# Kernel tuning notes

Measured on AMD Instinct MI355X. Metric: run time of the kernel, lower is better.

The kernel has to match this reference:

```python
import jax, jax.numpy as jnp
import numpy as np
import math

PI = math.pi
L = 6.0 * math.pi
EPS = 1e-5


def c19_activation(x, rho=4.0):
    scaled = x * (1.0 / PI)
    n = jnp.floor(scaled)
    t = scaled - n
    h = t * (1.0 - t)
    sgn = jnp.where(jnp.remainder(n, 2.0) < 1.0, 1.0, -1.0)
    core = PI * (sgn * h + rho * h * h)
    return jnp.where(x >= L, x - L, jnp.where(x <= -L, x + L, core))


def layer_norm(x, gamma, beta):
    mu = jnp.mean(x, axis=-1, keepdims=True)
    var = jnp.mean(jnp.square(x - mu), axis=-1, keepdims=True)
    return (x - mu) * jax.lax.rsqrt(var + EPS) * gamma + beta


def setup_inputs() -> dict:
    key = jax.random.key(0)
    ks = jax.random.split(key, 8)
    B, T, NB, D, DEPTH = 65536, 32, 8, 128, 4
    nl = DEPTH - 1  # 3 inner layers
    x = jax.random.normal(ks[0], (B, T, NB), dtype=jnp.float32)
    Wi = jax.random.normal(ks[1], (NB, D), dtype=jnp.float32) * 0.1   # input_proj (in, out)
    bi = jnp.zeros((D,), jnp.float32)
    Wo = jax.random.normal(ks[2], (D, NB), dtype=jnp.float32) * 0.1   # output_proj
    bo = jnp.zeros((NB,), jnp.float32)
    g_state = jnp.ones((D,), jnp.float32)
    b_state = jnp.zeros((D,), jnp.float32)
    Ws = jax.random.normal(ks[3], (nl, D, D), dtype=jnp.float32) * (1.0 / math.sqrt(D))
    bs = jnp.zeros((nl, D), jnp.float32)
    gs = jnp.ones((nl, D), jnp.float32)
    betas = jnp.zeros((nl, D), jnp.float32)
    return {"x": x, "Wi": Wi, "bi": bi, "Wo": Wo, "bo": bo,
            "g_state": g_state, "b_state": b_state,
            "Ws": Ws, "bs": bs, "gs": gs, "betas": betas}


def reference(x, Wi, bi, Wo, bo, g_state, b_state, Ws, bs, gs, betas):
    B, T, _ = x.shape
    D = Wi.shape[1]
    nl = Ws.shape[0]

    def step(h, xt):  # h: [B,D], xt: [B,NB]
        inp = xt @ Wi + bi
        state = 0.618 * layer_norm(h, g_state, b_state) + 0.382 * inp
        for i in range(nl):  # fixed small depth loop
            state = state + c19_activation(layer_norm(state, gs[i], betas[i]) @ Ws[i] + bs[i])
        out = state @ Wo + bo
        return state, out

    h0 = jnp.zeros((B, D), dtype=x.dtype)
    _, outs = jax.lax.scan(step, h0, jnp.swapaxes(x, 0, 1))  # outs: [T,B,NB]
    return jnp.swapaxes(outs, 0, 1)  # [B,T,NB]
```

## Files before the change

kernel.cpp:

```cpp
#include <hip/hip_runtime.h>
#include <math.h>

#define BDIM 512
#define BR   64
#define D    128
#define SPD  130
#define WSP  130
#define SWOP 12
#define TT   32
#define NB   8
#define NL   3

typedef double v4d __attribute__((ext_vector_type(4)));

__device__ __forceinline__ double c19_act_d(double x) {
    const double PI_D = 3.14159265358979323846;
    const double L6   = 6.0 * PI_D;
    double scaled = x * (1.0 / PI_D);
    double n = floor(scaled);
    double t = scaled - n;
    double h = t * (1.0 - t);
    double halfn = n * 0.5;
    double fr = halfn - floor(halfn);
    double sgn = (fr < 0.25) ? 1.0 : -1.0;
    double core = PI_D * (sgn * h + 4.0 * h * h);
    double r = core;
    r = (x <= -L6) ? (x + L6) : r;
    r = (x >=  L6) ? (x - L6) : r;
    return r;
}

__global__ void miniphi_prep(const float* __restrict__ Ws, const float* __restrict__ gs,
                             double* __restrict__ wp) {
    int idx = blockIdx.x * 256 + threadIdx.x;
    wp[idx] = (double)gs[idx >> 7] * (double)Ws[idx];
}

__global__ __launch_bounds__(BDIM) void miniphi_kernel(
    const float* __restrict__ x,  const float* __restrict__ Wi, const float* __restrict__ bi,
    const float* __restrict__ Wo, const float* __restrict__ bo,
    const float* __restrict__ g_state, const float* __restrict__ b_state,
    const float* __restrict__ Ws, const float* __restrict__ bs,
    const float* __restrict__ gs, const float* __restrict__ betas,
    const double* __restrict__ wp,
    float* __restrict__ out)
{
    __shared__ double sState[BR][SPD];
    __shared__ double sWq[2][32][WSP];
    __shared__ float  sWi[NB][D];
    __shared__ float  sWo[D][SWOP];
    __shared__ float  sBi[D], sGst[D], sBst[D];
    __shared__ double sGsD[NL][D];
    __shared__ double sGW[NL][D];
    __shared__ double sBWbs[NL][D];
    __shared__ double sRstd[BR], sMu2[BR];
    __shared__ float  sBo[NB];
    __shared__ int    sPR[64][4], sPC[64][4];
    __shared__ int    sFlag;

    const int tid  = threadIdx.x;
    const int lane = tid & 63;
    const int wv   = tid >> 6;

    for (int i = tid; i < NB * D; i += BDIM) sWi[i >> 7][i & 127] = Wi[i];
    for (int i = tid; i < D * NB; i += BDIM) sWo[i >> 3][i & 7] = Wo[i];
    for (int i = tid; i < D; i += BDIM) { sBi[i] = bi[i]; sGst[i] = g_state[i]; sBst[i] = b_state[i]; }
    for (int i = tid; i < NL * D; i += BDIM) sGsD[i >> 7][i & 127] = (double)gs[i];
    if (tid < NB) sBo[tid] = bo[tid];
    for (int i = tid; i < BR * D; i += BDIM) sState[i >> 7][i & 127] = 0.0;
    if (tid < NL * D) {
        int ly = tid >> 7, c = tid & 127;
        const float* wl = Ws + (size_t)ly * D * D;
        double gw = 0.0, bw = 0.0;
        for (int k = 0; k < D; ++k) {
            double w = (double)wl[k * D + c];
            gw = fma((double)gs[ly * D + k], w, gw);
            bw = fma((double)betas[ly * D + k], w, bw);
        }
        sGW[ly][c] = gw;
        sBWbs[ly][c] = bw + (double)bs[ly * D + c];
    }

    if (wv == 0) {
        const int lm = lane & 15, lk = lane >> 4;
        v4d z = {0.0, 0.0, 0.0, 0.0};
        v4d p1 = __builtin_amdgcn_mfma_f64_16x16x4f64((double)lm, 1.0, z, 0, 0, 0);
        v4d p2 = __builtin_amdgcn_mfma_f64_16x16x4f64(1.0, (double)lm, z, 0, 0, 0);
        double pk = (double)(1 << lk);
        v4d p3 = __builtin_amdgcn_mfma_f64_16x16x4f64(pk, pk, z, 0, 0, 0);
        v4d p4 = __builtin_amdgcn_mfma_f64_16x16x4f64(1.0 + 0x1p-30, 1.0, z, 0, 0, 0);
        double pa5 = (lk == 0) ? 1.0 : 0x1p-52;
        v4d p5 = __builtin_amdgcn_mfma_f64_16x16x4f64(pa5, 1.0, z, 0, 0, 0);
        bool ok = true;
        #pragma unroll
        for (int i = 0; i < 4; ++i) {
            double v = p1[i]; int r = (int)(v * 0.25 + 0.5);
            ok = ok && (v == 4.0 * (double)r) && (r >= 0) && (r < 16);
            sPR[lane][i] = r;
            double w = p2[i]; int c2 = (int)(w * 0.25 + 0.5);
            ok = ok && (w == 4.0 * (double)c2) && (c2 >= 0) && (c2 < 16);
            sPC[lane][i] = c2;
            ok = ok && (p3[i] == 85.0);
            ok = ok && (p4[i] == 4.0 + 0x1p-28);
            ok = ok && (p5[i] == 1.0 + 3.0 * 0x1p-52);
        }
        unsigned long long bal = __ballot(ok ? 1 : 0);
        if (lane == 0) sFlag = (bal == 0xFFFFFFFFFFFFFFFFull) ? 1 : 0;
    }
    __syncthreads();

    const int useMfma = sFlag;
    int pr[4], pc[4];
    #pragma unroll
    for (int i = 0; i < 4; ++i) { pr[i] = sPR[lane][i]; pc[i] = sPC[lane][i]; }

    const int rLN = tid >> 3;
    const int sL  = tid & 7;
    const int lm  = lane & 15, lk = lane >> 4;
    const int n0  = wv * 16;
    const int r0v = wv * 8;
    const size_t rowg = (size_t)blockIdx.x * BR;

    #define STAGE_Q(LY, Q, QB)                                                      \
      { if (wp) {                                                                   \
          const double* src = wp + (((size_t)(LY) * D + (Q) * 32) * D);             \
          _Pragma("unroll")                                                         \
          for (int i_ = 0; i_ < 4; ++i_) {                                          \
              int kr_ = wv * 4 + i_;                                                \
              const double* g_ = src + (size_t)kr_ * D + lane * 2;                  \
              __builtin_amdgcn_global_load_lds(                                     \
                  (const __attribute__((address_space(1))) void*)g_,                \
                  (__attribute__((address_space(3))) void*)&sWq[QB][kr_][0],        \
                  16, 0, 0);                                                        \
          }                                                                         \
        } else {                                                                    \
          const float* src = Ws + (((size_t)(LY) * D + (Q) * 32) * D);              \
          const double* gl = &sGsD[LY][(Q) * 32];                                   \
          _Pragma("unroll")                                                         \
          for (int i_ = 0; i_ < 4; ++i_) {                                          \
              int kr_ = wv * 4 + i_;                                                \
              float2 w_ = *(const float2*)(src + (size_t)kr_ * D + lane * 2);       \
              double g_ = gl[kr_];                                                  \
              double2 o_; o_.x = g_ * (double)w_.x; o_.y = g_ * (double)w_.y;       \
              *(double2*)&sWq[QB][kr_][lane * 2] = o_;                              \
          }                                                                         \
        } }

    #define GEMM_Q(QB, QK)                                                          \
      if (useMfma) {                                                                \
          _Pragma("unroll")                                                         \
          for (int k0 = 0; k0 < 32; k0 += 4) {                                      \
              double b  = sWq[QB][k0 + lk][n0 + lm];                                \
              double a0 = sState[lm     ][(QK) + k0 + lk];                          \
              double a1 = sState[lm + 16][(QK) + k0 + lk];                          \
              double a2 = sState[lm + 32][(QK) + k0 + lk];                          \
              double a3 = sState[lm + 48][(QK) + k0 + lk];                          \
              acc0 = __builtin_amdgcn_mfma_f64_16x16x4f64(a0, b, acc0, 0, 0, 0);    \
              acc1 = __builtin_amdgcn_mfma_f64_16x16x4f64(a1, b, acc1, 0, 0, 0);    \
              acc2 = __builtin_amdgcn_mfma_f64_16x16x4f64(a2, b, acc2, 0, 0, 0);    \
              acc3 = __builtin_amdgcn_mfma_f64_16x16x4f64(a3, b, acc3, 0, 0, 0);    \
          }                                                                         \
      } else {                                                                      \
          _Pragma("unroll 4")                                                       \
          for (int kk = 0; kk < 32; kk += 2) {                                      \
              int kg = (QK) + kk;                                                   \
              double b00 = sWq[QB][kk][lane],     b01 = sWq[QB][kk][lane + 64];     \
              double b10 = sWq[QB][kk + 1][lane], b11 = sWq[QB][kk + 1][lane + 64]; \
              _Pragma("unroll")                                                     \
              for (int r = 0; r < 8; ++r) {                                         \
                  double2 a = *(const double2*)&sState[r0v + r][kg];                \
                  accv[r][0] = fma(a.y, b10, fma(a.x, b00, accv[r][0]));            \
                  accv[r][1] = fma(a.y, b11, fma(a.x, b01, accv[r][1]));            \
              }                                                                     \
          }                                                                         \
      }

    STAGE_Q(0, 0, 0)

    for (int t = 0; t < TT; ++t) {
        {
            const float* xp = x + (rowg + (size_t)rLN) * (TT * NB) + (size_t)t * NB;
            float4 xa = *(const float4*)(xp);
            float4 xb = *(const float4*)(xp + 4);
            double xv[8] = {(double)xa.x, (double)xa.y, (double)xa.z, (double)xa.w,
                            (double)xb.x, (double)xb.y, (double)xb.z, (double)xb.w};
            double v[16];
            #pragma unroll
            for (int j = 0; j < 16; ++j) v[j] = sState[rLN][sL + 8 * j];
            double sum = 0.0;
            #pragma unroll
            for (int j = 0; j < 16; ++j) sum += v[j];
            sum += __shfl_xor(sum, 1); sum += __shfl_xor(sum, 2); sum += __shfl_xor(sum, 4);
            double mu = sum * (1.0 / 128.0);
            double sq = 0.0;
            #pragma unroll
            for (int j = 0; j < 16; ++j) { double dd = v[j] - mu; sq += dd * dd; }
            sq += __shfl_xor(sq, 1); sq += __shfl_xor(sq, 2); sq += __shfl_xor(sq, 4);
            double rstd = 1.0 / sqrt(sq * (1.0 / 128.0) + 1e-5);
            #pragma unroll
            for (int j = 0; j < 16; ++j) {
                int c = sL + 8 * j;
                double inp = (double)sBi[c];
                #pragma unroll
                for (int k = 0; k < 8; ++k)
                    inp = fma(xv[k], (double)sWi[k][c], inp);
                double ln = (v[j] - mu) * rstd * (double)sGst[c] + (double)sBst[c];
                sState[rLN][c] = 0.618 * ln + 0.382 * inp;
            }
        }
        __syncthreads();

        for (int ly = 0; ly < NL; ++ly) {
            v4d acc0 = {0,0,0,0}, acc1 = {0,0,0,0}, acc2 = {0,0,0,0}, acc3 = {0,0,0,0};
            double accv[8][2];
            #pragma unroll
            for (int r = 0; r < 8; ++r) { accv[r][0] = 0.0; accv[r][1] = 0.0; }

            STAGE_Q(ly, 1, 1)
            GEMM_Q(0, 0)
            {
                double sum = 0.0;
                #pragma unroll
                for (int j = 0; j < 16; ++j) sum += sState[rLN][sL + 8 * j];
                sum += __shfl_xor(sum, 1); sum += __shfl_xor(sum, 2); sum += __shfl_xor(sum, 4);
                double mu = sum * (1.0 / 128.0);
                double sq = 0.0;
                #pragma unroll
                for (int j = 0; j < 16; ++j) { double dd = sState[rLN][sL + 8 * j] - mu; sq += dd * dd; }
                sq += __shfl_xor(sq, 1); sq += __shfl_xor(sq, 2); sq += __shfl_xor(sq, 4);
                double rstd = 1.0 / sqrt(sq * (1.0 / 128.0) + 1e-5);
                if (sL == 0) { sRstd[rLN] = rstd; sMu2[rLN] = mu * rstd; }
            }
            __syncthreads();

            STAGE_Q(ly, 2, 0)
            GEMM_Q(1, 32)
            __syncthreads();

            STAGE_Q(ly, 3, 1)
            GEMM_Q(0, 64)
            __syncthreads();

            if (ly + 1 < NL) { STAGE_Q(ly + 1, 0, 0) } else { STAGE_Q(0, 0, 0) }
            GEMM_Q(1, 96)
            __syncthreads();

            if (useMfma) {
                #pragma unroll
                for (int i = 0; i < 4; ++i) {
                    int col = n0 + pc[i];
                    double gwc = sGW[ly][col], bwc = sBWbs[ly][col];
                    int R0 = pr[i];
                    double y0 = fma(sRstd[R0],      acc0[i], fma(-sMu2[R0],      gwc, bwc));
                    double y1 = fma(sRstd[R0 + 16], acc1[i], fma(-sMu2[R0 + 16], gwc, bwc));
                    double y2 = fma(sRstd[R0 + 32], acc2[i], fma(-sMu2[R0 + 32], gwc, bwc));
                    double y3 = fma(sRstd[R0 + 48], acc3[i], fma(-sMu2[R0 + 48], gwc, bwc));
                    sState[R0][col]      += c19_act_d(y0);
                    sState[R0 + 16][col] += c19_act_d(y1);
                    sState[R0 + 32][col] += c19_act_d(y2);
                    sState[R0 + 48][col] += c19_act_d(y3);
                }
            } else {
                double gwc0 = sGW[ly][lane],   gwc1 = sGW[ly][lane + 64];
                double bwc0 = sBWbs[ly][lane], bwc1 = sBWbs[ly][lane + 64];
                #pragma unroll
                for (int r = 0; r < 8; ++r) {
                    int R = r0v + r;
                    double rs = sRstd[R], m2 = sMu2[R];
                    double y0 = fma(rs, accv[r][0], fma(-m2, gwc0, bwc0));
                    double y1 = fma(rs, accv[r][1], fma(-m2, gwc1, bwc1));
                    sState[R][lane]      += c19_act_d(y0);
                    sState[R][lane + 64] += c19_act_d(y1);
                }
            }
            __syncthreads();
        }

        {
            double accj[8];
            #pragma unroll
            for (int j = 0; j < 8; ++j) accj[j] = 0.0;
            #pragma unroll
            for (int u = 0; u < 16; ++u) {
                int k = sL + 8 * u;
                double s = sState[rLN][k];
                float4 w0 = *(const float4*)&sWo[k][0];
                float4 w1 = *(const float4*)&sWo[k][4];
                accj[0] = fma(s, (double)w0.x, accj[0]);
                accj[1] = fma(s, (double)w0.y, accj[1]);
                accj[2] = fma(s, (double)w0.z, accj[2]);
                accj[3] = fma(s, (double)w0.w, accj[3]);
                accj[4] = fma(s, (double)w1.x, accj[4]);
                accj[5] = fma(s, (double)w1.y, accj[5]);
                accj[6] = fma(s, (double)w1.z, accj[6]);
                accj[7] = fma(s, (double)w1.w, accj[7]);
            }
            #pragma unroll
            for (int j = 0; j < 8; ++j) {
                accj[j] += __shfl_xor(accj[j], 1);
                accj[j] += __shfl_xor(accj[j], 2);
                accj[j] += __shfl_xor(accj[j], 4);
            }
            double o = accj[0];
            #pragma unroll
            for (int j = 1; j < 8; ++j) o = (sL == j) ? accj[j] : o;
            out[((rowg + (size_t)rLN) * TT + (size_t)t) * NB + sL] =
                (float)(o + (double)sBo[sL]);
        }
    }
    #undef GEMM_Q
    #undef STAGE_Q
}

extern "C" void kernel_launch(void* const* d_in, const int* in_sizes, int n_in,
                              void* d_out, int out_size, void* d_ws, size_t ws_size,
                              hipStream_t stream) {
    const float* x       = (const float*)d_in[0];
    const float* Wi      = (const float*)d_in[1];
    const float* bi      = (const float*)d_in[2];
    const float* Wo      = (const float*)d_in[3];
    const float* bo      = (const float*)d_in[4];
    const float* g_state = (const float*)d_in[5];
    const float* b_state = (const float*)d_in[6];
    const float* Ws      = (const float*)d_in[7];
    const float* bs      = (const float*)d_in[8];
    const float* gs      = (const float*)d_in[9];
    const float* betas   = (const float*)d_in[10];
    float* out = (float*)d_out;

    const size_t wp_bytes = (size_t)NL * D * D * sizeof(double);
    double* wp = (ws_size >= wp_bytes) ? (double*)d_ws : nullptr;
    if (wp) {
        dim3 pgrid(NL * D * D / 256), pblock(256);
        hipLaunchKernelGGL(miniphi_prep, pgrid, pblock, 0, stream, Ws, gs, wp);
    }

    const int B = in_sizes[0] / (TT * NB);
    dim3 grid(B / BR), block(BDIM);
    hipLaunchKernelGGL(miniphi_kernel, grid, block, 0, stream,
                       x, Wi, bi, Wo, bo, g_state, b_state, Ws, bs, gs, betas, wp, out);
}
```

Measured before the change: 5.208 ms.

## Double block size to 1024 threads and split row/column work across waves

Raises the threads per block from 512 to 1024 (16 waves). Each wave now owns a 32-row by 16-column MFMA tile instead of 64x16, and LayerNorm and output projection use 16 lanes per row instead of 8. Weight staging is spread over more waves. The aim is more latency hiding and parallelism per block, but it risks lower occupancy from register and LDS limits at 1024 threads, plus extra shuffle steps.

```diff
diff --git a/kernel.cpp b/kernel.cpp
--- a/kernel.cpp
+++ b/kernel.cpp
@@ -1,7 +1,7 @@
 #include <hip/hip_runtime.h>
 #include <math.h>
 
-#define BDIM 512
+#define BDIM 1024
 #define BR   64
 #define D    128
 #define SPD  130
@@ -114,19 +114,21 @@
     #pragma unroll
     for (int i = 0; i < 4; ++i) { pr[i] = sPR[lane][i]; pc[i] = sPC[lane][i]; }
 
-    const int rLN = tid >> 3;
-    const int sL  = tid & 7;
+    const int rLN = tid >> 4;
+    const int sL  = tid & 15;
     const int lm  = lane & 15, lk = lane >> 4;
-    const int n0  = wv * 16;
-    const int r0v = wv * 8;
+    const int rp  = wv >> 3;
+    const int rb  = rp * 32;
+    const int c0  = (wv & 7) * 16;
+    const int r0v = wv * 4;
     const size_t rowg = (size_t)blockIdx.x * BR;
 
     #define STAGE_Q(LY, Q, QB)                                                      \
       { if (wp) {                                                                   \
           const double* src = wp + (((size_t)(LY) * D + (Q) * 32) * D);             \
           _Pragma("unroll")                                                         \
-          for (int i_ = 0; i_ < 4; ++i_) {                                          \
-              int kr_ = wv * 4 + i_;                                                \
+          for (int i_ = 0; i_ < 2; ++i_) {                                          \
+              int kr_ = wv * 2 + i_;                                                \
               const double* g_ = src + (size_t)kr_ * D + lane * 2;                  \
               __builtin_amdgcn_global_load_lds(                                     \
                   (const __attribute__((address_space(1))) void*)g_,                \
@@ -137,8 +139,8 @@
           const float* src = Ws + (((size_t)(LY) * D + (Q) * 32) * D);              \
           const double* gl = &sGsD[LY][(Q) * 32];                                   \
           _Pragma("unroll")                                                         \
-          for (int i_ = 0; i_ < 4; ++i_) {                                          \
-              int kr_ = wv * 4 + i_;                                                \
+          for (int i_ = 0; i_ < 2; ++i_) {                                          \
+              int kr_ = wv * 2 + i_;                                                \
               float2 w_ = *(const float2*)(src + (size_t)kr_ * D + lane * 2);       \
               double g_ = gl[kr_];                                                  \
               double2 o_; o_.x = g_ * (double)w_.x; o_.y = g_ * (double)w_.y;       \
@@ -150,15 +152,11 @@
       if (useMfma) {                                                                \
           _Pragma("unroll")                                                         \
           for (int k0 = 0; k0 < 32; k0 += 4) {                                      \
-              double b  = sWq[QB][k0 + lk][n0 + lm];                                \
-              double a0 = sState[lm     ][(QK) + k0 + lk];                          \
-              double a1 = sState[lm + 16][(QK) + k0 + lk];                          \
-              double a2 = sState[lm + 32][(QK) + k0 + lk];                          \
-              double a3 = sState[lm + 48][(QK) + k0 + lk];                          \
+              double b  = sWq[QB][k0 + lk][c0 + lm];                                \
+              double a0 = sState[rb + lm     ][(QK) + k0 + lk];                     \
+              double a1 = sState[rb + lm + 16][(QK) + k0 + lk];                     \
               acc0 = __builtin_amdgcn_mfma_f64_16x16x4f64(a0, b, acc0, 0, 0, 0);    \
               acc1 = __builtin_amdgcn_mfma_f64_16x16x4f64(a1, b, acc1, 0, 0, 0);    \
-              acc2 = __builtin_amdgcn_mfma_f64_16x16x4f64(a2, b, acc2, 0, 0, 0);    \
-              acc3 = __builtin_amdgcn_mfma_f64_16x16x4f64(a3, b, acc3, 0, 0, 0);    \
           }                                                                         \
       } else {                                                                      \
           _Pragma("unroll 4")                                                       \
@@ -167,7 +165,7 @@
               double b00 = sWq[QB][kk][lane],     b01 = sWq[QB][kk][lane + 64];     \
               double b10 = sWq[QB][kk + 1][lane], b11 = sWq[QB][kk + 1][lane + 64]; \
               _Pragma("unroll")                                                     \
-              for (int r = 0; r < 8; ++r) {                                         \
+              for (int r = 0; r < 4; ++r) {                                         \
                   double2 a = *(const double2*)&sState[r0v + r][kg];                \
                   accv[r][0] = fma(a.y, b10, fma(a.x, b00, accv[r][0]));            \
                   accv[r][1] = fma(a.y, b11, fma(a.x, b01, accv[r][1]));            \
@@ -184,22 +182,24 @@
             float4 xb = *(const float4*)(xp + 4);
             double xv[8] = {(double)xa.x, (double)xa.y, (double)xa.z, (double)xa.w,
                             (double)xb.x, (double)xb.y, (double)xb.z, (double)xb.w};
-            double v[16];
-            #pragma unroll
-            for (int j = 0; j < 16; ++j) v[j] = sState[rLN][sL + 8 * j];
+            double v[8];
+            #pragma unroll
+            for (int j = 0; j < 8; ++j) v[j] = sState[rLN][sL + 16 * j];
             double sum = 0.0;
             #pragma unroll
-            for (int j = 0; j < 16; ++j) sum += v[j];
-            sum += __shfl_xor(sum, 1); sum += __shfl_xor(sum, 2); sum += __shfl_xor(sum, 4);
+            for (int j = 0; j < 8; ++j) sum += v[j];
+            sum += __shfl_xor(sum, 1); sum += __shfl_xor(sum, 2);
+            sum += __shfl_xor(sum, 4); sum += __shfl_xor(sum, 8);
             double mu = sum * (1.0 / 128.0);
             double sq = 0.0;
             #pragma unroll
-            for (int j = 0; j < 16; ++j) { double dd = v[j] - mu; sq += dd * dd; }
-            sq += __shfl_xor(sq, 1); sq += __shfl_xor(sq, 2); sq += __shfl_xor(sq, 4);
+            for (int j = 0; j < 8; ++j) { double dd = v[j] - mu; sq += dd * dd; }
+            sq += __shfl_xor(sq, 1); sq += __shfl_xor(sq, 2);
+            sq += __shfl_xor(sq, 4); sq += __shfl_xor(sq, 8);
             double rstd = 1.0 / sqrt(sq * (1.0 / 128.0) + 1e-5);
             #pragma unroll
-            for (int j = 0; j < 16; ++j) {
-                int c = sL + 8 * j;
+            for (int j = 0; j < 8; ++j) {
+                int c = sL + 16 * j;
                 double inp = (double)sBi[c];
                 #pragma unroll
                 for (int k = 0; k < 8; ++k)
@@ -211,23 +211,25 @@
         __syncthreads();
 
         for (int ly = 0; ly < NL; ++ly) {
-            v4d acc0 = {0,0,0,0}, acc1 = {0,0,0,0}, acc2 = {0,0,0,0}, acc3 = {0,0,0,0};
-            double accv[8][2];
-            #pragma unroll
-            for (int r = 0; r < 8; ++r) { accv[r][0] = 0.0; accv[r][1] = 0.0; }
+            v4d acc0 = {0,0,0,0}, acc1 = {0,0,0,0};
+            double accv[4][2];
+            #pragma unroll
+            for (int r = 0; r < 4; ++r) { accv[r][0] = 0.0; accv[r][1] = 0.0; }
 
             STAGE_Q(ly, 1, 1)
             GEMM_Q(0, 0)
             {
                 double sum = 0.0;
                 #pragma unroll
-                for (int j = 0; j < 16; ++j) sum += sState[rLN][sL + 8 * j];
-                sum += __shfl_xor(sum, 1); sum += __shfl_xor(sum, 2); sum += __shfl_xor(sum, 4);
+                for (int j = 0; j < 8; ++j) sum += sState[rLN][sL + 16 * j];
+                sum += __shfl_xor(sum, 1); sum += __shfl_xor(sum, 2);
+                sum += __shfl_xor(sum, 4); sum += __shfl_xor(sum, 8);
                 double mu = sum * (1.0 / 128.0);
                 double sq = 0.0;
                 #pragma unroll
-                for (int j = 0; j < 16; ++j) { double dd = sState[rLN][sL + 8 * j] - mu; sq += dd * dd; }
-                sq += __shfl_xor(sq, 1); sq += __shfl_xor(sq, 2); sq += __shfl_xor(sq, 4);
+                for (int j = 0; j < 8; ++j) { double dd = sState[rLN][sL + 16 * j] - mu; sq += dd * dd; }
+                sq += __shfl_xor(sq, 1); sq += __shfl_xor(sq, 2);
+                sq += __shfl_xor(sq, 4); sq += __shfl_xor(sq, 8);
                 double rstd = 1.0 / sqrt(sq * (1.0 / 128.0) + 1e-5);
                 if (sL == 0) { sRstd[rLN] = rstd; sMu2[rLN] = mu * rstd; }
             }
@@ -248,23 +250,19 @@
             if (useMfma) {
                 #pragma unroll
                 for (int i = 0; i < 4; ++i) {
-                    int col = n0 + pc[i];
+                    int col = c0 + pc[i];
                     double gwc = sGW[ly][col], bwc = sBWbs[ly][col];
-                    int R0 = pr[i];
+                    int R0 = rb + pr[i];
                     double y0 = fma(sRstd[R0],      acc0[i], fma(-sMu2[R0],      gwc, bwc));
                     double y1 = fma(sRstd[R0 + 16], acc1[i], fma(-sMu2[R0 + 16], gwc, bwc));
-                    double y2 = fma(sRstd[R0 + 32], acc2[i], fma(-sMu2[R0 + 32], gwc, bwc));
-                    double y3 = fma(sRstd[R0 + 48], acc3[i], fma(-sMu2[R0 + 48], gwc, bwc));
                     sState[R0][col]      += c19_act_d(y0);
                     sState[R0 + 16][col] += c19_act_d(y1);
-                    sState[R0 + 32][col] += c19_act_d(y2);
-                    sState[R0 + 48][col] += c19_act_d(y3);
                 }
             } else {
                 double gwc0 = sGW[ly][lane],   gwc1 = sGW[ly][lane + 64];
                 double bwc0 = sBWbs[ly][lane], bwc1 = sBWbs[ly][lane + 64];
                 #pragma unroll
-                for (int r = 0; r < 8; ++r) {
+                for (int r = 0; r < 4; ++r) {
                     int R = r0v + r;
                     double rs = sRstd[R], m2 = sMu2[R];
                     double y0 = fma(rs, accv[r][0], fma(-m2, gwc0, bwc0));
@@ -281,8 +279,8 @@
             #pragma unroll
             for (int j = 0; j < 8; ++j) accj[j] = 0.0;
             #pragma unroll
-            for (int u = 0; u < 16; ++u) {
-                int k = sL + 8 * u;
+            for (int u = 0; u < 8; ++u) {
+                int k = sL + 16 * u;
                 double s = sState[rLN][k];
                 float4 w0 = *(const float4*)&sWo[k][0];
                 float4 w1 = *(const float4*)&sWo[k][4];
@@ -300,12 +298,14 @@
                 accj[j] += __shfl_xor(accj[j], 1);
                 accj[j] += __shfl_xor(accj[j], 2);
                 accj[j] += __shfl_xor(accj[j], 4);
+                accj[j] += __shfl_xor(accj[j], 8);
             }
             double o = accj[0];
             #pragma unroll
             for (int j = 1; j < 8; ++j) o = (sL == j) ? accj[j] : o;
-            out[((rowg + (size_t)rLN) * TT + (size_t)t) * NB + sL] =
-                (float)(o + (double)sBo[sL]);
+            if (sL < NB)
+                out[((rowg + (size_t)rLN) * TT + (size_t)t) * NB + sL] =
+                    (float)(o + (double)sBo[sL]);
         }
     }
     #undef GEMM_Q
```

Result: no change. 5.146 ms (-1.2%).
